# Optimization experiments

Measured on AMD Instinct MI355X. Metric: run time of the kernel, lower is better.

## Reference

```python
import jax, jax.numpy as jnp
import numpy as np

DIM, N_HEADS, N_EXPERTS, TOP_K = 1024, 16, 8, 2
D_FF = 4 * DIM
HEAD_DIM = DIM // N_HEADS
EPS = 1e-5


def layer_norm(x, g, b):
    m = x.mean(-1, keepdims=True)
    v = ((x - m) ** 2).mean(-1, keepdims=True)
    return (x - m) / jnp.sqrt(v + EPS) * g + b


def setup_inputs() -> dict:
    key = jax.random.key(0)
    ks = jax.random.split(key, 16)
    B, T = 8, 1024
    s = 0.02
    inp = {
        'x': jax.random.normal(ks[0], (B, T, DIM), jnp.float32),
        'attention_mask': jnp.ones((B, T), jnp.int32),
        'Wq': jax.random.normal(ks[1], (DIM, DIM), jnp.float32) * s,
        'bq': jnp.zeros((DIM,), jnp.float32),
        'Wk': jax.random.normal(ks[2], (DIM, DIM), jnp.float32) * s,
        'bk': jnp.zeros((DIM,), jnp.float32),
        'Wv': jax.random.normal(ks[3], (DIM, DIM), jnp.float32) * s,
        'bv': jnp.zeros((DIM,), jnp.float32),
        'Wo': jax.random.normal(ks[4], (DIM, DIM), jnp.float32) * s,
        'bo': jnp.zeros((DIM,), jnp.float32),
        'g1': jnp.ones((DIM,), jnp.float32),
        'beta1': jnp.zeros((DIM,), jnp.float32),
        'router_w': jax.random.normal(ks[5], (DIM, N_EXPERTS), jnp.float32) * s,
        'router_b': jnp.zeros((N_EXPERTS,), jnp.float32),
        'W1': jax.random.normal(ks[6], (N_EXPERTS, DIM, D_FF), jnp.float32) * s,
        'B1': jnp.zeros((N_EXPERTS, D_FF), jnp.float32),
        'W2': jax.random.normal(ks[7], (N_EXPERTS, D_FF, DIM), jnp.float32) * s,
        'B2': jnp.zeros((N_EXPERTS, DIM), jnp.float32),
        'g2': jnp.ones((DIM,), jnp.float32),
        'beta2': jnp.zeros((DIM,), jnp.float32),
    }
    return inp


def reference(x, attention_mask, Wq, bq, Wk, bk, Wv, bv, Wo, bo, g1, beta1,
              router_w, router_b, W1, B1, W2, B2, g2, beta2):
    B, T, D = x.shape
    H, hd = N_HEADS, HEAD_DIM
    # ---- multi-head attention with causal + padding mask ----
    q = (x @ Wq + bq).reshape(B, T, H, hd).transpose(0, 2, 1, 3)  # [B,H,T,hd]
    k = (x @ Wk + bk).reshape(B, T, H, hd).transpose(0, 2, 1, 3)
    v = (x @ Wv + bv).reshape(B, T, H, hd).transpose(0, 2, 1, 3)
    scores = jnp.einsum('bhqd,bhkd->bhqk', q, k) / jnp.sqrt(jnp.float32(hd))
    causal = jnp.tril(jnp.ones((T, T), bool))[None, None]            # [1,1,T,T]
    mask = causal & (attention_mask[:, None, None, :] != 0)         # [B,1,T,T]
    scores = jnp.where(mask, scores, jnp.float32(-1e9))
    attn = jax.nn.softmax(scores, axis=-1)
    h = jnp.einsum('bhqk,bhkd->bhqd', attn, v).transpose(0, 2, 1, 3).reshape(B, T, D)
    h = h @ Wo + bo
    # dropout is identity in eval mode
    x1 = layer_norm(x + h, g1, beta1)
    # ---- sparse top-k MoE FFN ----
    xf = x1.reshape(-1, D)                                           # [N,D]
    logits = xf @ router_w + router_b                                # [N,E]
    probs = jax.nn.softmax(logits, axis=-1)
    topv, topi = jax.lax.top_k(probs, TOP_K)                         # [N,k]
    gk = topv / topv.sum(-1, keepdims=True)                          # renormalized gates
    onehot = jax.nn.one_hot(topi, N_EXPERTS, dtype=xf.dtype)         # [N,k,E]
    gates = (onehot * gk[..., None]).sum(1)                          # [N,E]
    y = jnp.zeros_like(xf)
    for e in range(N_EXPERTS):  # fixed small expert loop
        he = jax.nn.relu(xf @ W1[e] + B1[e])
        y = y + gates[:, e:e + 1] * (he @ W2[e] + B2[e])
    # load-balancing loss: E * sum_i f_i * P_i
    f = onehot.sum(1).mean(0)                                        # fraction routed per expert
    P = probs.mean(0)
    lb = jnp.float32(N_EXPERTS) * (f * P).sum()
    out = layer_norm(x1 + y.reshape(B, T, D), g2, beta2)
    return out, lb
```

## Files before the change

### kernel.cpp

```cpp
#include <hip/hip_runtime.h>
#include <hip/hip_bf16.h>
#include <stdint.h>

#define DIMQ   1024
#define NHEADS 16
#define HD     64
#define NEXP   8
#define DFF    4096
#define NTOK   8192
#define TSEQ   1024
#define BATCH  8

typedef unsigned short u16;
typedef unsigned int   u32;
typedef __attribute__((ext_vector_type(8))) short bf16x8;
typedef __attribute__((ext_vector_type(4))) float f32x4;

__device__ __forceinline__ float bf_lo(u32 w) { return __uint_as_float(w << 16); }
__device__ __forceinline__ float bf_hi(u32 w) { return __uint_as_float(w & 0xffff0000u); }
__device__ __forceinline__ u16 f2bf(float f) {
  u32 x = __float_as_uint(f);
  return (u16)((x + 0x7fffu + ((x >> 16) & 1u)) >> 16);
}

__device__ __forceinline__ void gload16(const u16* g, u16* l) {
  __builtin_amdgcn_global_load_lds((const __attribute__((address_space(1))) u32*)g,
                                   (__attribute__((address_space(3))) u32*)l, 16, 0, 0);
}

__global__ __launch_bounds__(256) void cvt_f32_bf16(const float* __restrict__ in,
                                                    u16* __restrict__ out, int n) {
  int i = (blockIdx.x * 256 + threadIdx.x) * 4;
  if (i >= n) return;
  float4 v = *(const float4*)(in + i);
  ushort4 o;
  o.x = f2bf(v.x); o.y = f2bf(v.y); o.z = f2bf(v.z); o.w = f2bf(v.w);
  *(ushort4*)(out + i) = o;
}

__global__ __launch_bounds__(256) void transpose_f32_bf16(
    const float* __restrict__ in, u16* __restrict__ out, int R, int C) {
  __shared__ float tile[32][33];
  size_t base = (size_t)blockIdx.z * (size_t)R * (size_t)C;
  int tx = threadIdx.x & 31, ty = threadIdx.x >> 5;
  int c = blockIdx.x * 32 + tx;
#pragma unroll
  for (int i = 0; i < 4; i++) {
    int r = blockIdx.y * 32 + ty + i * 8;
    tile[ty + i * 8][tx] = in[base + (size_t)r * C + c];
  }
  __syncthreads();
  int rr = blockIdx.y * 32 + tx;
#pragma unroll
  for (int i = 0; i < 4; i++) {
    int cc = blockIdx.x * 32 + ty + i * 8;
    out[base + (size_t)cc * R + rr] = f2bf(tile[tx][ty + i * 8]);
  }
}

template <bool GATHER, bool RELU, bool TRANSC>
__device__ __forceinline__ void gemm_core(
    const u16* __restrict__ A, const u16* __restrict__ Bt,
    const float* __restrict__ bias, u16* __restrict__ C,
    int M, int N, int K, const int* __restrict__ gidx) {
  __shared__ u16 As[128 * 32];
  __shared__ u16 Bs[128 * 32];
  const int tid = threadIdx.x;
  const int lane = tid & 63;
  const int wave = tid >> 6;
  const int wr = wave >> 1, wc = wave & 1;
  const int lr = lane & 15, kg = lane >> 4;
  const int rowbase = blockIdx.y * 128;
  const int colbase = blockIdx.x * 128;

  f32x4 acc[4][4];
#pragma unroll
  for (int m = 0; m < 4; m++)
#pragma unroll
    for (int n = 0; n < 4; n++) acc[m][n] = (f32x4){0.f, 0.f, 0.f, 0.f};

  const int r0 = tid >> 2, seg = tid & 3;
  const int slog = seg ^ ((r0 >> 1) & 3);
  int ar0 = rowbase + r0;      if (ar0 >= M) ar0 = M - 1;
  int ar1 = rowbase + r0 + 64; if (ar1 >= M) ar1 = M - 1;
  const long arow0 = GATHER ? gidx[ar0] : ar0;
  const long arow1 = GATHER ? gidx[ar1] : ar1;
  const u16* Aptr0 = A + (size_t)arow0 * K + slog * 8;
  const u16* Aptr1 = A + (size_t)arow1 * K + slog * 8;
  const u16* Bptr0 = Bt + (size_t)(colbase + r0) * K + slog * 8;
  const u16* Bptr1 = Bt + (size_t)(colbase + r0 + 64) * K + slog * 8;
  u16* ldsA0 = &As[tid * 8];
  u16* ldsA1 = &As[2048 + tid * 8];
  u16* ldsB0 = &Bs[tid * 8];
  u16* ldsB1 = &Bs[2048 + tid * 8];

  const int swz = (lr >> 1) & 3;

  for (int k0 = 0; k0 < K; k0 += 32) {
    gload16(Aptr0 + k0, ldsA0);
    gload16(Aptr1 + k0, ldsA1);
    gload16(Bptr0 + k0, ldsB0);
    gload16(Bptr1 + k0, ldsB1);
    __syncthreads();
    bf16x8 af[4], bfr[4];
#pragma unroll
    for (int m = 0; m < 4; m++)
      af[m] = *(const bf16x8*)(&As[(wr * 64 + m * 16 + lr) * 32 + ((kg ^ swz) * 8)]);
#pragma unroll
    for (int n = 0; n < 4; n++)
      bfr[n] = *(const bf16x8*)(&Bs[(wc * 64 + n * 16 + lr) * 32 + ((kg ^ swz) * 8)]);
#pragma unroll
    for (int m = 0; m < 4; m++)
#pragma unroll
      for (int n = 0; n < 4; n++)
        acc[m][n] = __builtin_amdgcn_mfma_f32_16x16x32_bf16(af[m], bfr[n], acc[m][n], 0, 0, 0);
    __syncthreads();
  }
#pragma unroll
  for (int n = 0; n < 4; n++) {
    int col = colbase + wc * 64 + n * 16 + lr;
    float bv = bias[col];
#pragma unroll
    for (int m = 0; m < 4; m++) {
      int row0 = rowbase + wr * 64 + m * 16 + kg * 4;
      if (TRANSC) {
        if (row0 + 3 < M) {
          ushort4 pk;
          pk.x = f2bf(acc[m][n][0] + bv);
          pk.y = f2bf(acc[m][n][1] + bv);
          pk.z = f2bf(acc[m][n][2] + bv);
          pk.w = f2bf(acc[m][n][3] + bv);
          *(ushort4*)(&C[(size_t)col * M + row0]) = pk;
        } else {
#pragma unroll
          for (int r = 0; r < 4; r++)
            if (row0 + r < M) C[(size_t)col * M + row0 + r] = f2bf(acc[m][n][r] + bv);
        }
      } else {
#pragma unroll
        for (int r = 0; r < 4; r++) {
          int row = row0 + r;
          if (row < M) {
            float v = acc[m][n][r] + bv;
            if (RELU) v = fmaxf(v, 0.f);
            C[(size_t)row * N + col] = f2bf(v);
          }
        }
      }
    }
  }
}

__global__ __launch_bounds__(256) void gemm_bt_kernel(
    const u16* __restrict__ A, const u16* __restrict__ Bt,
    const float* __restrict__ bias, u16* __restrict__ C, int M, int N, int K) {
  gemm_core<false, false, false>(A, Bt, bias, C, M, N, K, nullptr);
}

__global__ __launch_bounds__(256) void gemm_bt_tc_kernel(
    const u16* __restrict__ A, const u16* __restrict__ Bt,
    const float* __restrict__ bias, u16* __restrict__ C, int M, int N, int K) {
  gemm_core<false, false, true>(A, Bt, bias, C, M, N, K, nullptr);
}

__global__ __launch_bounds__(256) void moe_gemm1_kernel(
    const u16* __restrict__ x1b, const u16* __restrict__ W1t,
    const float* __restrict__ B1, u16* __restrict__ he,
    const int* __restrict__ cnt, const int* __restrict__ off,
    const int* __restrict__ idxlist) {
  int e = blockIdx.z;
  int M = cnt[e];
  if ((int)blockIdx.y * 128 >= M) return;
  gemm_core<true, true, false>(x1b, W1t + (size_t)e * DFF * DIMQ, B1 + e * DFF,
                               he + (size_t)off[e] * DFF, M, DFF, DIMQ, idxlist + off[e]);
}

__global__ __launch_bounds__(256) void moe_gemm2_kernel(
    const u16* __restrict__ he, const u16* __restrict__ W2t,
    const float* __restrict__ B2, u16* __restrict__ yslot,
    const int* __restrict__ cnt, const int* __restrict__ off) {
  int e = blockIdx.z;
  int M = cnt[e];
  if ((int)blockIdx.y * 128 >= M) return;
  gemm_core<false, false, false>(he + (size_t)off[e] * DFF, W2t + (size_t)e * DIMQ * DFF,
                                 B2 + e * DIMQ, yslot + (size_t)off[e] * DIMQ, M, DIMQ, DFF, nullptr);
}

__global__ __launch_bounds__(256) void attn_mfma_kernel(
    const u16* __restrict__ qb, const u16* __restrict__ kb,
    const u16* __restrict__ vbT, const int* __restrict__ amask,
    u16* __restrict__ hb) {
  __shared__ u16 Ks[32 * 64];
  __shared__ u16 VTs[64 * 32];
  __shared__ u16 Ps[4][16 * 32];
  __shared__ float mbias[32];

  const int b = blockIdx.y >> 4;
  const int h = blockIdx.y & 15;
  const int qb0 = blockIdx.x * 64;
  const int tid = threadIdx.x;
  const int lane = tid & 63;
  const int wq = tid >> 6;
  const int r16 = lane & 15;
  const int kg = lane >> 4;
  const int qrow0 = qb0 + wq * 16;

  bf16x8 qf[2];
  {
    const u16* qp = qb + ((size_t)(b * TSEQ + qrow0 + r16)) * DIMQ + h * HD + kg * 8;
    qf[0] = *(const bf16x8*)(qp);
    qf[1] = *(const bf16x8*)(qp + 32);
  }
  f32x4 acc[4];
#pragma unroll
  for (int db = 0; db < 4; db++) acc[db] = (f32x4){0.f, 0.f, 0.f, 0.f};
  float m_run[4], l_run[4];
#pragma unroll
  for (int i = 0; i < 4; i++) { m_run[i] = -3.0e38f; l_run[i] = 0.f; }

  const int skey = tid >> 3, sslot = tid & 7;
  const int sd = tid >> 2, sko = tid & 3;
  const u16* kgb = kb + (size_t)(b * TSEQ) * DIMQ + h * HD;
  const u16* vgb = vbT + (size_t)(h * HD) * NTOK + (size_t)b * TSEQ;

  const int nt = (qb0 + 64) >> 5;
  for (int kt = 0; kt < nt; kt++) {
    const int k0g = kt * 32;
    __syncthreads();
    {
      uint4 kv = *(const uint4*)(kgb + (size_t)(k0g + skey) * DIMQ + sslot * 8);
      *(uint4*)(&Ks[skey * 64 + ((sslot ^ (skey & 7)) * 8)]) = kv;
      uint4 vv = *(const uint4*)(vgb + (size_t)sd * NTOK + k0g + sko * 8);
      *(uint4*)(&VTs[sd * 32 + ((sko ^ (sd & 3)) * 8)]) = vv;
      if (tid < 32) mbias[tid] = amask[b * TSEQ + k0g + tid] ? 0.f : -1e9f;
    }
    __syncthreads();
    if (k0g < qrow0 + 16) {
      f32x4 s0 = (f32x4){0.f, 0.f, 0.f, 0.f};
      f32x4 s1 = (f32x4){0.f, 0.f, 0.f, 0.f};
      {
        int key0 = r16;
        bf16x8 ka = *(const bf16x8*)(&Ks[key0 * 64 + ((kg ^ (key0 & 7)) * 8)]);
        bf16x8 kb2 = *(const bf16x8*)(&Ks[key0 * 64 + (((4 + kg) ^ (key0 & 7)) * 8)]);
        s0 = __builtin_amdgcn_mfma_f32_16x16x32_bf16(qf[0], ka, s0, 0, 0, 0);
        s0 = __builtin_amdgcn_mfma_f32_16x16x32_bf16(qf[1], kb2, s0, 0, 0, 0);
        int key1 = 16 + r16;
        bf16x8 kc = *(const bf16x8*)(&Ks[key1 * 64 + ((kg ^ (key1 & 7)) * 8)]);
        bf16x8 kd = *(const bf16x8*)(&Ks[key1 * 64 + (((4 + kg) ^ (key1 & 7)) * 8)]);
        s1 = __builtin_amdgcn_mfma_f32_16x16x32_bf16(qf[0], kc, s1, 0, 0, 0);
        s1 = __builtin_amdgcn_mfma_f32_16x16x32_bf16(qf[1], kd, s1, 0, 0, 0);
      }
      float sv0[4], sv1[4], tm[4];
      float mb0 = mbias[r16], mb1 = mbias[16 + r16];
#pragma unroll
      for (int i = 0; i < 4; i++) {
        int qg = qrow0 + kg * 4 + i;
        float a = s0[i] * 0.125f + mb0;
        float c = s1[i] * 0.125f + mb1;
        if (k0g + r16 > qg)      a = -3.0e38f;
        if (k0g + 16 + r16 > qg) c = -3.0e38f;
        sv0[i] = a; sv1[i] = c;
        tm[i] = fmaxf(a, c);
      }
#pragma unroll
      for (int mk = 1; mk < 16; mk <<= 1) {
#pragma unroll
        for (int i = 0; i < 4; i++) tm[i] = fmaxf(tm[i], __shfl_xor(tm[i], mk));
      }
      float pr0[4], pr1[4];
#pragma unroll
      for (int i = 0; i < 4; i++) {
        float nm = fmaxf(m_run[i], tm[i]);
        float sc = __expf(m_run[i] - nm);
        m_run[i] = nm;
        pr0[i] = __expf(sv0[i] - nm);
        pr1[i] = __expf(sv1[i] - nm);
        l_run[i] = l_run[i] * sc + pr0[i] + pr1[i];
#pragma unroll
        for (int db = 0; db < 4; db++) acc[db][i] *= sc;
      }
#pragma unroll
      for (int i = 0; i < 4; i++) {
        int qrl = kg * 4 + i;
        int sw = qrl & 3;
        Ps[wq][qrl * 32 + (((r16 >> 3) ^ sw) * 8) + (r16 & 7)] = f2bf(pr0[i]);
        Ps[wq][qrl * 32 + ((((16 + r16) >> 3) ^ sw) * 8) + (r16 & 7)] = f2bf(pr1[i]);
      }
      bf16x8 pf = *(const bf16x8*)(&Ps[wq][r16 * 32 + ((kg ^ (r16 & 3)) * 8)]);
#pragma unroll
      for (int db = 0; db < 4; db++) {
        int d = db * 16 + r16;
        bf16x8 vf = *(const bf16x8*)(&VTs[d * 32 + ((kg ^ (d & 3)) * 8)]);
        acc[db] = __builtin_amdgcn_mfma_f32_16x16x32_bf16(pf, vf, acc[db], 0, 0, 0);
      }
    }
  }
#pragma unroll
  for (int mk = 1; mk < 16; mk <<= 1) {
#pragma unroll
    for (int i = 0; i < 4; i++) l_run[i] += __shfl_xor(l_run[i], mk);
  }
#pragma unroll
  for (int i = 0; i < 4; i++) {
    float inv = 1.f / l_run[i];
    int qg = qrow0 + kg * 4 + i;
    u16* op = hb + ((size_t)(b * TSEQ + qg)) * DIMQ + h * HD + r16;
#pragma unroll
    for (int db = 0; db < 4; db++) op[db * 16] = f2bf(acc[db][i] * inv);
  }
}

__global__ __launch_bounds__(256) void addln_kernel(
    const float* __restrict__ xin, const u16* __restrict__ hres,
    const float* __restrict__ g, const float* __restrict__ beta,
    float* __restrict__ x1, u16* __restrict__ x1b) {
  __shared__ float red[8];
  int t = blockIdx.x;
  int d = threadIdx.x * 4;
  size_t base = (size_t)t * DIMQ + d;
  float4 xv = *(const float4*)(xin + base);
  uint2 hu = *(const uint2*)(hres + base);
  float v0 = xv.x + bf_lo(hu.x), v1 = xv.y + bf_hi(hu.x);
  float v2 = xv.z + bf_lo(hu.y), v3 = xv.w + bf_hi(hu.y);
  float s1 = v0 + v1 + v2 + v3;
  float s2 = v0 * v0 + v1 * v1 + v2 * v2 + v3 * v3;
#pragma unroll
  for (int off = 32; off; off >>= 1) {
    s1 += __shfl_down(s1, off);
    s2 += __shfl_down(s2, off);
  }
  int w = threadIdx.x >> 6;
  if ((threadIdx.x & 63) == 0) { red[w] = s1; red[4 + w] = s2; }
  __syncthreads();
  float S1 = red[0] + red[1] + red[2] + red[3];
  float S2 = red[4] + red[5] + red[6] + red[7];
  float m = S1 * (1.f / DIMQ);
  float var = S2 * (1.f / DIMQ) - m * m;
  float rs = rsqrtf(var + 1e-5f);
  float4 gv = *(const float4*)(g + d);
  float4 bv = *(const float4*)(beta + d);
  float o0 = (v0 - m) * rs * gv.x + bv.x;
  float o1 = (v1 - m) * rs * gv.y + bv.y;
  float o2 = (v2 - m) * rs * gv.z + bv.z;
  float o3 = (v3 - m) * rs * gv.w + bv.w;
  *(float4*)(x1 + base) = make_float4(o0, o1, o2, o3);
  uint2 pu;
  pu.x = (u32)f2bf(o0) | ((u32)f2bf(o1) << 16);
  pu.y = (u32)f2bf(o2) | ((u32)f2bf(o3) << 16);
  *(uint2*)(x1b + base) = pu;
}

__global__ __launch_bounds__(256) void router_kernel(
    const float* __restrict__ x1, const float* __restrict__ rw,
    const float* __restrict__ rb, int* __restrict__ topi,
    float* __restrict__ gkout, float* __restrict__ probs) {
  int t = blockIdx.x * 4 + (threadIdx.x >> 6);
  int l = threadIdx.x & 63;
  float acc[8];
#pragma unroll
  for (int e = 0; e < 8; e++) acc[e] = 0.f;
  const float* xr = x1 + (size_t)t * DIMQ;
  for (int k = l; k < DIMQ; k += 64) {
    float xv = xr[k];
    const float* w = rw + (size_t)k * 8;
#pragma unroll
    for (int e = 0; e < 8; e++) acc[e] += xv * w[e];
  }
#pragma unroll
  for (int e = 0; e < 8; e++) {
#pragma unroll
    for (int off = 32; off; off >>= 1) acc[e] += __shfl_down(acc[e], off);
  }
  if (l == 0) {
    float lg[8], p[8];
    float mx = -3e38f;
#pragma unroll
    for (int e = 0; e < 8; e++) { lg[e] = acc[e] + rb[e]; mx = fmaxf(mx, lg[e]); }
    float sum = 0.f;
#pragma unroll
    for (int e = 0; e < 8; e++) { p[e] = expf(lg[e] - mx); sum += p[e]; }
    float isum = 1.f / sum;
#pragma unroll
    for (int e = 0; e < 8; e++) p[e] *= isum;
    int e0 = 0;
#pragma unroll
    for (int e = 1; e < 8; e++) if (p[e] > p[e0]) e0 = e;
    int e1 = (e0 == 0) ? 1 : 0;
#pragma unroll
    for (int e = 0; e < 8; e++) if (e != e0 && p[e] > p[e1]) e1 = e;
    float s2 = p[e0] + p[e1];
    topi[2 * t] = e0; topi[2 * t + 1] = e1;
    gkout[2 * t] = p[e0] / s2; gkout[2 * t + 1] = p[e1] / s2;
    float* pp = probs + (size_t)t * 8;
#pragma unroll
    for (int e = 0; e < 8; e++) pp[e] = p[e];
  }
}

__global__ __launch_bounds__(256) void stats_kernel(
    const float* __restrict__ probs, const int* __restrict__ topi,
    int* __restrict__ cnt, float* __restrict__ Psum) {
  __shared__ float sps[4][8];
  __shared__ int   slc[4][8];
  float ps[8];
  int lc[8];
#pragma unroll
  for (int e = 0; e < 8; e++) { ps[e] = 0.f; lc[e] = 0; }
  int t = blockIdx.x * 256 + threadIdx.x;
  {
    const float* p = probs + (size_t)t * 8;
#pragma unroll
    for (int e = 0; e < 8; e++) ps[e] += p[e];
    lc[topi[2 * t]]++;
    lc[topi[2 * t + 1]]++;
  }
#pragma unroll
  for (int e = 0; e < 8; e++) {
#pragma unroll
    for (int off = 32; off; off >>= 1) {
      ps[e] += __shfl_down(ps[e], off);
      lc[e] += __shfl_down(lc[e], off);
    }
  }
  int w = threadIdx.x >> 6;
  if ((threadIdx.x & 63) == 0) {
#pragma unroll
    for (int e = 0; e < 8; e++) { sps[w][e] = ps[e]; slc[w][e] = lc[e]; }
  }
  __syncthreads();
  if (threadIdx.x < 8) {
    float fp = sps[0][threadIdx.x] + sps[1][threadIdx.x] + sps[2][threadIdx.x] + sps[3][threadIdx.x];
    int   fc = slc[0][threadIdx.x] + slc[1][threadIdx.x] + slc[2][threadIdx.x] + slc[3][threadIdx.x];
    atomicAdd(&Psum[threadIdx.x], fp);
    atomicAdd(&cnt[threadIdx.x], fc);
  }
}

__global__ void offsets_kernel(const int* __restrict__ cnt, const float* __restrict__ Psum,
                               int* __restrict__ off, int* __restrict__ fill,
                               float* __restrict__ lb_out) {
  if (threadIdx.x == 0 && blockIdx.x == 0) {
    int o = 0;
    float lb = 0.f;
    for (int e = 0; e < NEXP; e++) {
      off[e] = o;
      fill[e] = o;
      o += cnt[e];
      lb += ((float)cnt[e] / (float)NTOK) * (Psum[e] / (float)NTOK);
    }
    lb_out[0] = (float)NEXP * lb;
  }
}

__global__ __launch_bounds__(256) void listbuild_kernel(
    const int* __restrict__ topi, int* fill, int* __restrict__ idxlist,
    int* __restrict__ posmap) {
  __shared__ int bcnt[8];
  __shared__ int base[8];
  __shared__ int bofs[8];
  int t = blockIdx.x * 256 + threadIdx.x;
  if (threadIdx.x < 8) { bcnt[threadIdx.x] = 0; bofs[threadIdx.x] = 0; }
  __syncthreads();
  int e0 = topi[2 * t], e1 = topi[2 * t + 1];
  atomicAdd(&bcnt[e0], 1);
  atomicAdd(&bcnt[e1], 1);
  __syncthreads();
  if (threadIdx.x < 8) base[threadIdx.x] = atomicAdd(&fill[threadIdx.x], bcnt[threadIdx.x]);
  __syncthreads();
  int s0 = base[e0] + atomicAdd(&bofs[e0], 1);
  idxlist[s0] = t;
  posmap[2 * t] = s0;
  int s1 = base[e1] + atomicAdd(&bofs[e1], 1);
  idxlist[s1] = t;
  posmap[2 * t + 1] = s1;
}

__global__ __launch_bounds__(256) void finalln_kernel(
    const float* __restrict__ x1, const u16* __restrict__ yslot,
    const int* __restrict__ posmap, const float* __restrict__ gkv,
    const float* __restrict__ g, const float* __restrict__ beta,
    float* __restrict__ out) {
  __shared__ float red[8];
  int t = blockIdx.x;
  int p0 = posmap[2 * t], p1 = posmap[2 * t + 1];
  float g0 = gkv[2 * t], g1 = gkv[2 * t + 1];
  int d = threadIdx.x * 4;
  size_t base = (size_t)t * DIMQ + d;
  float4 xv = *(const float4*)(x1 + base);
  uint2 y0 = *(const uint2*)(yslot + (size_t)p0 * DIMQ + d);
  uint2 y1 = *(const uint2*)(yslot + (size_t)p1 * DIMQ + d);
  float v0 = xv.x + g0 * bf_lo(y0.x) + g1 * bf_lo(y1.x);
  float v1 = xv.y + g0 * bf_hi(y0.x) + g1 * bf_hi(y1.x);
  float v2 = xv.z + g0 * bf_lo(y0.y) + g1 * bf_lo(y1.y);
  float v3 = xv.w + g0 * bf_hi(y0.y) + g1 * bf_hi(y1.y);
  float s1 = v0 + v1 + v2 + v3;
  float s2 = v0 * v0 + v1 * v1 + v2 * v2 + v3 * v3;
#pragma unroll
  for (int off = 32; off; off >>= 1) {
    s1 += __shfl_down(s1, off);
    s2 += __shfl_down(s2, off);
  }
  int w = threadIdx.x >> 6;
  if ((threadIdx.x & 63) == 0) { red[w] = s1; red[4 + w] = s2; }
  __syncthreads();
  float S1 = red[0] + red[1] + red[2] + red[3];
  float S2 = red[4] + red[5] + red[6] + red[7];
  float m = S1 * (1.f / DIMQ);
  float var = S2 * (1.f / DIMQ) - m * m;
  float rs = rsqrtf(var + 1e-5f);
  float4 gv = *(const float4*)(g + d);
  float4 bv = *(const float4*)(beta + d);
  float4 o;
  o.x = (v0 - m) * rs * gv.x + bv.x;
  o.y = (v1 - m) * rs * gv.y + bv.y;
  o.z = (v2 - m) * rs * gv.z + bv.z;
  o.w = (v3 - m) * rs * gv.w + bv.w;
  *(float4*)(out + base) = o;
}

extern "C" void kernel_launch(void* const* d_in, const int* in_sizes, int n_in,
                              void* d_out, int out_size, void* d_ws, size_t ws_size,
                              hipStream_t stream) {
  const float* x     = (const float*)d_in[0];
  const int*   amask = (const int*)d_in[1];
  const float* Wq    = (const float*)d_in[2];
  const float* bq    = (const float*)d_in[3];
  const float* Wk    = (const float*)d_in[4];
  const float* bk    = (const float*)d_in[5];
  const float* Wv    = (const float*)d_in[6];
  const float* bv    = (const float*)d_in[7];
  const float* Wo    = (const float*)d_in[8];
  const float* bo    = (const float*)d_in[9];
  const float* g1    = (const float*)d_in[10];
  const float* beta1 = (const float*)d_in[11];
  const float* rw    = (const float*)d_in[12];
  const float* rb    = (const float*)d_in[13];
  const float* W1    = (const float*)d_in[14];
  const float* B1    = (const float*)d_in[15];
  const float* W2    = (const float*)d_in[16];
  const float* B2    = (const float*)d_in[17];
  const float* g2    = (const float*)d_in[18];
  const float* beta2 = (const float*)d_in[19];
  float* out    = (float*)d_out;
  float* lb_out = out + (size_t)NTOK * DIMQ;

  char* ws = (char*)d_ws;
  size_t off_acc = 0;
  auto alloc = [&](size_t bytes) {
    void* p = ws + off_acc;
    off_acc += (bytes + 255) & ~(size_t)255;
    return p;
  };
  u16* xb    = (u16*)alloc((size_t)NTOK * DIMQ * 2);
  u16* qbuf  = (u16*)alloc((size_t)NTOK * DIMQ * 2);
  u16* kbuf  = (u16*)alloc((size_t)NTOK * DIMQ * 2);
  u16* vbufT = (u16*)alloc((size_t)NTOK * DIMQ * 2);
  u16* hb    = (u16*)alloc((size_t)NTOK * DIMQ * 2);
  u16* ho    = (u16*)alloc((size_t)NTOK * DIMQ * 2);
  float* x1  = (float*)alloc((size_t)NTOK * DIMQ * 4);
  u16* x1b   = (u16*)alloc((size_t)NTOK * DIMQ * 2);
  u16* Wqt   = (u16*)alloc((size_t)DIMQ * DIMQ * 2);
  u16* Wkt   = (u16*)alloc((size_t)DIMQ * DIMQ * 2);
  u16* Wvt   = (u16*)alloc((size_t)DIMQ * DIMQ * 2);
  u16* Wot   = (u16*)alloc((size_t)DIMQ * DIMQ * 2);
  u16* W1t   = (u16*)alloc((size_t)NEXP * DFF * DIMQ * 2);
  u16* W2t   = (u16*)alloc((size_t)NEXP * DIMQ * DFF * 2);
  u16* he    = (u16*)alloc((size_t)2 * NTOK * DFF * 2);
  u16* yslot = (u16*)alloc((size_t)2 * NTOK * DIMQ * 2);
  char* stats = (char*)alloc(4096);
  int*   cnt   = (int*)stats;
  float* Psum  = (float*)(stats + 32);
  int*   offp  = (int*)(stats + 64);
  int*   fill  = (int*)(stats + 96);
  int* topi    = (int*)alloc((size_t)NTOK * 2 * 4);
  float* gkbuf = (float*)alloc((size_t)NTOK * 2 * 4);
  int* posmap  = (int*)alloc((size_t)NTOK * 2 * 4);
  int* idxlist = (int*)alloc((size_t)NTOK * 2 * 4);
  float* probs = (float*)alloc((size_t)NTOK * 8 * 4);

  hipMemsetAsync(stats, 0, 64, stream);

  cvt_f32_bf16<<<NTOK * DIMQ / 1024, 256, 0, stream>>>(x, xb, NTOK * DIMQ);
  transpose_f32_bf16<<<dim3(DIMQ / 32, DIMQ / 32, 1), 256, 0, stream>>>(Wq, Wqt, DIMQ, DIMQ);
  transpose_f32_bf16<<<dim3(DIMQ / 32, DIMQ / 32, 1), 256, 0, stream>>>(Wk, Wkt, DIMQ, DIMQ);
  transpose_f32_bf16<<<dim3(DIMQ / 32, DIMQ / 32, 1), 256, 0, stream>>>(Wv, Wvt, DIMQ, DIMQ);
  transpose_f32_bf16<<<dim3(DIMQ / 32, DIMQ / 32, 1), 256, 0, stream>>>(Wo, Wot, DIMQ, DIMQ);
  transpose_f32_bf16<<<dim3(DFF / 32, DIMQ / 32, NEXP), 256, 0, stream>>>(W1, W1t, DIMQ, DFF);
  transpose_f32_bf16<<<dim3(DIMQ / 32, DFF / 32, NEXP), 256, 0, stream>>>(W2, W2t, DFF, DIMQ);

  dim3 gproj(DIMQ / 128, NTOK / 128);
  gemm_bt_kernel<<<gproj, 256, 0, stream>>>(xb, Wqt, bq, qbuf, NTOK, DIMQ, DIMQ);
  gemm_bt_kernel<<<gproj, 256, 0, stream>>>(xb, Wkt, bk, kbuf, NTOK, DIMQ, DIMQ);
  gemm_bt_tc_kernel<<<gproj, 256, 0, stream>>>(xb, Wvt, bv, vbufT, NTOK, DIMQ, DIMQ);
  attn_mfma_kernel<<<dim3(TSEQ / 64, BATCH * NHEADS), 256, 0, stream>>>(qbuf, kbuf, vbufT, amask, hb);
  gemm_bt_kernel<<<gproj, 256, 0, stream>>>(hb, Wot, bo, ho, NTOK, DIMQ, DIMQ);
  addln_kernel<<<NTOK, 256, 0, stream>>>(x, ho, g1, beta1, x1, x1b);

  router_kernel<<<NTOK / 4, 256, 0, stream>>>(x1, rw, rb, topi, gkbuf, probs);
  stats_kernel<<<NTOK / 256, 256, 0, stream>>>(probs, topi, cnt, Psum);
  offsets_kernel<<<1, 64, 0, stream>>>(cnt, Psum, offp, fill, lb_out);
  listbuild_kernel<<<NTOK / 256, 256, 0, stream>>>(topi, fill, idxlist, posmap);
  moe_gemm1_kernel<<<dim3(DFF / 128, NTOK / 128, NEXP), 256, 0, stream>>>(x1b, W1t, B1, he, cnt, offp, idxlist);
  moe_gemm2_kernel<<<dim3(DIMQ / 128, NTOK / 128, NEXP), 256, 0, stream>>>(he, W2t, B2, yslot, cnt, offp);
  finalln_kernel<<<NTOK, 256, 0, stream>>>(x1, yslot, posmap, gkbuf, g2, beta2, out);
}
```

Before: 934.4 us.

## Use 256x256 tiled 512-thread GEMM core for MoE expert GEMMs

```diff
diff --git a/kernel.cpp b/kernel.cpp
--- a/kernel.cpp
+++ b/kernel.cpp
@@ -163,27 +163,119 @@
   gemm_core<false, false, true>(A, Bt, bias, C, M, N, K, nullptr);
 }
 
-__global__ __launch_bounds__(256) void moe_gemm1_kernel(
+template <bool GATHER, bool RELU>
+__device__ __forceinline__ void gemm256_core(
+    const u16* __restrict__ A, const u16* __restrict__ Bt,
+    const float* __restrict__ bias, u16* __restrict__ C,
+    int M, int N, int K, const int* __restrict__ gidx) {
+  __shared__ u16 lds[2][2][256 * 64];
+  const int tid = threadIdx.x;
+  const int lane = tid & 63;
+  const int wave = tid >> 6;
+  const int wr = wave >> 2;
+  const int wcol = wave & 3;
+  const int lr = lane & 15, kg = lane >> 4;
+  const int rowbase = blockIdx.y * 256;
+  const int colbase = blockIdx.x * 256;
+
+  f32x4 acc[8][4];
+#pragma unroll
+  for (int m = 0; m < 8; m++)
+#pragma unroll
+    for (int n = 0; n < 4; n++) acc[m][n] = (f32x4){0.f, 0.f, 0.f, 0.f};
+
+  const int srow0 = tid >> 3, sphys = tid & 7;
+  const u16* asrc[4];
+  const u16* bsrc[4];
+#pragma unroll
+  for (int j = 0; j < 4; j++) {
+    int row = srow0 + j * 64;
+    int ls = sphys ^ (row & 7);
+    int ar = rowbase + row; if (ar >= M) ar = M - 1;
+    long ga = GATHER ? gidx[ar] : ar;
+    asrc[j] = A + (size_t)ga * K + ls * 8;
+    bsrc[j] = Bt + (size_t)(colbase + row) * K + ls * 8;
+  }
+
+#define STAGE256(buf, k0)                                              \
+  {                                                                    \
+    _Pragma("unroll")                                                  \
+    for (int j = 0; j < 4; j++) {                                      \
+      gload16(asrc[j] + (k0), &lds[buf][0][tid * 8 + j * 4096]);       \
+      gload16(bsrc[j] + (k0), &lds[buf][1][tid * 8 + j * 4096]);       \
+    }                                                                  \
+  }
+
+  STAGE256(0, 0);
+  __syncthreads();
+  const int NT = K >> 6;
+  for (int t = 0; t < NT; t++) {
+    const int buf = t & 1;
+    if (t + 1 < NT) STAGE256(buf ^ 1, (t + 1) << 6);
+    bf16x8 bfr[4][2];
+#pragma unroll
+    for (int nr = 0; nr < 4; nr++) {
+      int rb = wcol * 64 + nr * 16 + lr;
+#pragma unroll
+      for (int kk = 0; kk < 2; kk++)
+        bfr[nr][kk] = *(const bf16x8*)(&lds[buf][1][rb * 64 + (((kk * 4 + kg) ^ (rb & 7)) * 8)]);
+    }
+#pragma unroll
+    for (int mr = 0; mr < 8; mr++) {
+      int ra = wr * 128 + mr * 16 + lr;
+      bf16x8 a0 = *(const bf16x8*)(&lds[buf][0][ra * 64 + ((kg ^ (ra & 7)) * 8)]);
+      bf16x8 a1 = *(const bf16x8*)(&lds[buf][0][ra * 64 + (((4 + kg) ^ (ra & 7)) * 8)]);
+#pragma unroll
+      for (int nr = 0; nr < 4; nr++) {
+        acc[mr][nr] = __builtin_amdgcn_mfma_f32_16x16x32_bf16(a0, bfr[nr][0], acc[mr][nr], 0, 0, 0);
+        acc[mr][nr] = __builtin_amdgcn_mfma_f32_16x16x32_bf16(a1, bfr[nr][1], acc[mr][nr], 0, 0, 0);
+      }
+    }
+    __syncthreads();
+  }
+#undef STAGE256
+
+#pragma unroll
+  for (int nr = 0; nr < 4; nr++) {
+    int col = colbase + wcol * 64 + nr * 16 + lr;
+    float bv = bias[col];
+#pragma unroll
+    for (int mr = 0; mr < 8; mr++) {
+      int row0 = rowbase + wr * 128 + mr * 16 + kg * 4;
+#pragma unroll
+      for (int r = 0; r < 4; r++) {
+        int row = row0 + r;
+        if (row < M) {
+          float v = acc[mr][nr][r] + bv;
+          if (RELU) v = fmaxf(v, 0.f);
+          C[(size_t)row * N + col] = f2bf(v);
+        }
+      }
+    }
+  }
+}
+
+__global__ __launch_bounds__(512, 2) void moe_gemm1_kernel(
     const u16* __restrict__ x1b, const u16* __restrict__ W1t,
     const float* __restrict__ B1, u16* __restrict__ he,
     const int* __restrict__ cnt, const int* __restrict__ off,
     const int* __restrict__ idxlist) {
   int e = blockIdx.z;
   int M = cnt[e];
-  if ((int)blockIdx.y * 128 >= M) return;
-  gemm_core<true, true, false>(x1b, W1t + (size_t)e * DFF * DIMQ, B1 + e * DFF,
-                               he + (size_t)off[e] * DFF, M, DFF, DIMQ, idxlist + off[e]);
-}
-
-__global__ __launch_bounds__(256) void moe_gemm2_kernel(
+  if ((int)blockIdx.y * 256 >= M) return;
+  gemm256_core<true, true>(x1b, W1t + (size_t)e * DFF * DIMQ, B1 + e * DFF,
+                           he + (size_t)off[e] * DFF, M, DFF, DIMQ, idxlist + off[e]);
+}
+
+__global__ __launch_bounds__(512, 2) void moe_gemm2_kernel(
     const u16* __restrict__ he, const u16* __restrict__ W2t,
     const float* __restrict__ B2, u16* __restrict__ yslot,
     const int* __restrict__ cnt, const int* __restrict__ off) {
   int e = blockIdx.z;
   int M = cnt[e];
-  if ((int)blockIdx.y * 128 >= M) return;
-  gemm_core<false, false, false>(he + (size_t)off[e] * DFF, W2t + (size_t)e * DIMQ * DFF,
-                                 B2 + e * DIMQ, yslot + (size_t)off[e] * DIMQ, M, DIMQ, DFF, nullptr);
+  if ((int)blockIdx.y * 256 >= M) return;
+  gemm256_core<false, false>(he + (size_t)off[e] * DFF, W2t + (size_t)e * DIMQ * DFF,
+                             B2 + e * DIMQ, yslot + (size_t)off[e] * DIMQ, M, DIMQ, DFF, nullptr);
 }
 
 __global__ __launch_bounds__(256) void attn_mfma_kernel(
@@ -600,7 +692,7 @@
   stats_kernel<<<NTOK / 256, 256, 0, stream>>>(probs, topi, cnt, Psum);
   offsets_kernel<<<1, 64, 0, stream>>>(cnt, Psum, offp, fill, lb_out);
   listbuild_kernel<<<NTOK / 256, 256, 0, stream>>>(topi, fill, idxlist, posmap);
-  moe_gemm1_kernel<<<dim3(DFF / 128, NTOK / 128, NEXP), 256, 0, stream>>>(x1b, W1t, B1, he, cnt, offp, idxlist);
-  moe_gemm2_kernel<<<dim3(DIMQ / 128, NTOK / 128, NEXP), 256, 0, stream>>>(he, W2t, B2, yslot, cnt, offp);
+  moe_gemm1_kernel<<<dim3(DFF / 256, 32, NEXP), 512, 0, stream>>>(x1b, W1t, B1, he, cnt, offp, idxlist);
+  moe_gemm2_kernel<<<dim3(DIMQ / 256, 32, NEXP), 512, 0, stream>>>(he, W2t, B2, yslot, cnt, offp);
   finalln_kernel<<<NTOK, 256, 0, stream>>>(x1, yslot, posmap, gkbuf, g2, beta2, out);
 }
```

Measured after the change: 898.4 us. -3.9%, faster.
